# Optimization experiments

Hardware: AMD Instinct MI355X
Metric: run time of the kernel (lower is better)

The kernel has to match this reference:

```python
import jax, jax.numpy as jnp
import numpy as np

G, N, F, H, E = 3, 40000, 256, 128, 640000


def gcn_conv(x, W, b, edge_index):
    """PyG GCNConv: x @ W, add self-loops, sym-normalized scatter-add, + bias."""
    n = x.shape[0]
    x = x @ W
    loop = jnp.arange(n)
    row = jnp.concatenate([edge_index[0], loop])  # source nodes
    col = jnp.concatenate([edge_index[1], loop])  # target nodes
    deg = jax.ops.segment_sum(jnp.ones_like(row, dtype=x.dtype), col, num_segments=n)
    dinv = jnp.where(deg > 0, jax.lax.rsqrt(jnp.maximum(deg, 1e-12)), 0.0)
    norm = dinv[row] * dinv[col]
    out = jax.ops.segment_sum(x[row] * norm[:, None], col, num_segments=n)
    return out + b


def setup_inputs() -> dict:
    key = jax.random.key(0)
    ks = jax.random.split(key, 14)
    inp = {
        'x': jax.random.normal(ks[0], (G, N, F), jnp.float32),
        'edge_index': jax.random.randint(ks[1], (G, 2, E), 0, N, jnp.int64),
        'fc1_W': jax.random.normal(ks[2], (G, F, H), jnp.float32) * 0.05,
        'fc1_b': jax.random.normal(ks[3], (G, H), jnp.float32) * 0.05,
        'conv1_W': jax.random.normal(ks[4], (G, H, H), jnp.float32) * 0.05,
        'conv1_b': jax.random.normal(ks[5], (G, H), jnp.float32) * 0.05,
        'conv2_W': jax.random.normal(ks[6], (G, H, H), jnp.float32) * 0.05,
        'conv2_b': jax.random.normal(ks[7], (G, H), jnp.float32) * 0.05,
        'dconv1_W': jax.random.normal(ks[8], (G, H, H), jnp.float32) * 0.05,
        'dconv1_b': jax.random.normal(ks[9], (G, H), jnp.float32) * 0.05,
        'dconv2_W': jax.random.normal(ks[10], (G, H, H), jnp.float32) * 0.05,
        'dconv2_b': jax.random.normal(ks[11], (G, H), jnp.float32) * 0.05,
        'fc2_W': jax.random.normal(ks[12], (H, F), jnp.float32) * 0.05,
        'fc2_b': jax.random.normal(ks[13], (F,), jnp.float32) * 0.05,
    }
    return inp


def reference(x, edge_index, fc1_W, fc1_b, conv1_W, conv1_b, conv2_W, conv2_b,
              dconv1_W, dconv1_b, dconv2_W, dconv2_b, fc2_W, fc2_b):
    def encoder(xi, ei, fw, fb, c1w, c1b, c2w, c2b):
        pre = xi @ fw + fb                     # fc1
        h = gcn_conv(pre, c1w, c1b, ei)
        h = gcn_conv(h, c2w, c2b, ei)
        return pre, jax.nn.relu(h)

    pre_feat, enc = jax.vmap(encoder)(x, edge_index, fc1_W, fc1_b,
                                      conv1_W, conv1_b, conv2_W, conv2_b)

    # Faithful reproduction of the sequentially-mutating cross-graph block.
    h = [enc[i] for i in range(G)]
    for i in range(G):
        for j in range(G):
            if j != i:
                h[i] = h[i] + h[j]
        h[i] = h[G - 1] - h[i]  # loop var j ends at G-1 (zeroes tensor when i==G-1)
        h[i] = gcn_conv(h[i], dconv1_W[i], dconv1_b[i], edge_index[i])
        h[i] = gcn_conv(h[i], dconv2_W[i], dconv2_b[i], edge_index[i])

    fin_feat = h[0]
    for k in range(1, G - 1):
        fin_feat = fin_feat + h[k]

    loss_embedding = jax.nn.softmax(fin_feat @ fc2_W + fc2_b, axis=-1)
    return pre_feat, enc, jnp.stack(h), fin_feat, loss_embedding
```

## Files before the change

### kernel.cpp

```cpp
#include <hip/hip_runtime.h>
#include <hip/hip_bf16.h>

#define NV 40000
#define FD 256
#define HD 128
#define ED 640000
#define NG 3
#define NH (NV*HD)

#define CH  64
#define EPC (ED/CH)
#define NB  625

typedef unsigned short u16;
typedef unsigned int   u32;
typedef __attribute__((ext_vector_type(8))) u16    u16x8;
typedef __attribute__((ext_vector_type(8))) __bf16 bf16x8;
typedef __attribute__((ext_vector_type(4))) float  f32x4;

__device__ inline u16 f2b(float f){ __bf16 h = (__bf16)f; return __builtin_bit_cast(u16, h); }
__device__ inline float b2f(u16 u){ u32 x = ((u32)u)<<16; return __builtin_bit_cast(float, x); }
__device__ inline void acc2(u32 w, float&a, float&b){
  a += __builtin_bit_cast(float, w<<16);
  b += __builtin_bit_cast(float, w & 0xFFFF0000u);
}

__device__ inline void tr_seg(const float* __restrict__ src, u16* __restrict__ dst,
                              int K, int NN, long idx, long total){
  if (idx>=total) return;
  long per=(long)K*NN; long mat=idx/per; long rem=idx-mat*per;
  int k=(int)(rem/NN), c=(int)(rem-(long)k*NN);
  dst[mat*per+(long)c*K+k]=f2b(src[idx]);
}

__global__ __launch_bounds__(256) void htr_k(
    const int* __restrict__ ei, int* __restrict__ btot,
    const float* fc1W, const float* fc2W,
    const float* c1W, const float* c2W, const float* c1b,
    const float* d1W, const float* d2W, const float* d1b,
    u16* w_fc1, u16* w_fc2, u16* w_ce, u16* w_cd,
    float* t_enc, float* t_dec)
{
  __shared__ int h[NB];
  int b = blockIdx.x, t = threadIdx.x;
  if (b < 192){
    int ch = b % CH, g = b / CH;
    for (int i=t;i<NB;i+=256) h[i]=0;
    __syncthreads();
    const int* cc = ei + (long)g*2*ED + ED + ch*EPC;
    for (int j=t;j<EPC;j+=256) atomicAdd(&h[cc[j]>>6],1);
    __syncthreads();
    for (int bb=t;bb<NB;bb+=256){ int v=h[bb]; if(v) atomicAdd(&btot[g*NB+bb], v); }
    return;
  }
  int blk = b - 192;
  if (blk < 384){
    tr_seg(fc1W, w_fc1, FD, HD, (long)blk*256+t, (long)NG*FD*HD);
  } else if (blk < 512){
    tr_seg(fc2W, w_fc2, HD, FD, (long)(blk-384)*256+t, (long)HD*FD);
  } else if (blk < 832){
    int bb=blk-512;
    int mat=bb>>6;
    int local=(bb&63)*256+t;
    int n=local>>7, k=local&127;
    const float* W1; const float* W2; u16* dst;
    if (mat<3){ W1=c1W+(long)mat*HD*HD; W2=c2W+(long)mat*HD*HD; dst=w_ce+(long)mat*HD*HD; }
    else { int md=mat-3; W1=d1W+(long)md*HD*HD; W2=d2W+(long)md*HD*HD; dst=w_cd+(long)md*HD*HD; }
    float s=0.f;
    for (int j=0;j<HD;j++) s += W1[k*HD+j]*W2[j*HD+n];
    dst[(long)n*HD+k]=f2b(s);
  } else {
    for (int idx=t; idx<768; idx+=256){
      int which=idx>>7, n=idx&127;
      const float* bv; const float* W; float* dst;
      if (which<3){ bv=c1b+which*HD; W=c2W+(long)which*HD*HD; dst=t_enc+which*HD; }
      else { int w2=which-3; bv=d1b+w2*HD; W=d2W+(long)w2*HD*HD; dst=t_dec+w2*HD; }
      float s=0.f;
      for (int k=0;k<HD;k++) s += bv[k]*W[(long)k*HD+n];
      dst[n]=s;
    }
  }
}

__global__ void scanB_k(const int* __restrict__ btot, int* __restrict__ base, int* __restrict__ gcur){
  __shared__ int wsum[16];
  int tid=threadIdx.x, lane=tid&63, wv=tid>>6;
  for (int g=0; g<NG; ++g){
    int v = (tid<NB)? btot[g*NB+tid] : 0;
    int s=v;
    #pragma unroll
    for (int d=1; d<64; d<<=1){ int u=__shfl_up(s,d,64); if(lane>=d) s+=u; }
    if (lane==63) wsum[wv]=s;
    __syncthreads();
    if (wv==0){
      int t3=(lane<16)?wsum[lane]:0;
      #pragma unroll
      for (int d=1; d<16; d<<=1){ int u=__shfl_up(t3,d,64); if(lane>=d) t3+=u; }
      if (lane<16) wsum[lane]=t3;
    }
    __syncthreads();
    int incl = s + (wv>0? wsum[wv-1]:0);
    if (tid<NB){
      base[g*(NB+1)+tid]=incl-v;
      gcur[g*NB+tid]=incl-v;
      if (tid==NB-1) base[g*(NB+1)+NB]=incl;
    }
    __syncthreads();
  }
}

__global__ __launch_bounds__(256) void scat_k(const int* __restrict__ ei, int* __restrict__ gcur,
                                              u32* __restrict__ temp){
  int ch=blockIdx.x, g=blockIdx.y, t=threadIdx.x;
  __shared__ int h[NB];
  __shared__ int cur[NB];
  for (int i=t;i<NB;i+=256) h[i]=0;
  __syncthreads();
  const int* rr = ei + (long)g*2*ED + ch*EPC;
  const int* cc = rr + ED;
  for (int j=t;j<EPC;j+=256) atomicAdd(&h[cc[j]>>6],1);
  __syncthreads();
  for (int b=t;b<NB;b+=256){ int v=h[b]; cur[b] = v? atomicAdd(&gcur[g*NB+b], v) : 0; }
  __syncthreads();
  u32* tg = temp + (long)g*ED;
  for (int j=t;j<EPC;j+=256){
    int r=rr[j], c=cc[j];
    int pos=atomicAdd(&cur[c>>6],1);
    tg[pos]=((u32)(c&63)<<16)|(u32)r;
  }
}

__global__ __launch_bounds__(256) void sort_k(const u32* __restrict__ temp, const int* __restrict__ base,
                                              u16* __restrict__ csr, int* __restrict__ cptr,
                                              float* __restrict__ dinv){
  int b=blockIdx.x, g=blockIdx.y, t=threadIdx.x;
  __shared__ int cnt[64];
  __shared__ int cur[64];
  if (t<64) cnt[t]=0;
  __syncthreads();
  const u32* tg = temp + (long)g*ED;
  int s=base[g*(NB+1)+b], e=base[g*(NB+1)+b+1];
  for (int i=s+t;i<e;i+=256) atomicAdd(&cnt[tg[i]>>16],1);
  __syncthreads();
  if (t<64){
    int v=cnt[t];
    int sc=v;
    #pragma unroll
    for (int d=1;d<64;d<<=1){ int u=__shfl_up(sc,d,64); if(t>=d) sc+=u; }
    int st = s + sc - v;
    cur[t]=st;
    cptr[(long)g*(NV+1) + b*64 + t] = st;
    if (b==NB-1 && t==63) cptr[(long)g*(NV+1)+NV] = e;
    dinv[(long)g*NV + b*64 + t] = rsqrtf((float)v+1.0f);
  }
  __syncthreads();
  u16* cg = csr + (long)g*ED;
  for (int i=s+t;i<e;i+=256){
    u32 tt=tg[i];
    int pos=atomicAdd(&cur[tt>>16],1);
    cg[pos]=(u16)(tt&0xFFFF);
  }
}

__device__ __forceinline__ void agg_body(
    const u16* __restrict__ xw, const u16* __restrict__ csr,
    const int* __restrict__ cptr, const float* __restrict__ dinv,
    u16* __restrict__ outB, int c, int lane, int scOut)
{
  const uint2* xp2 = (const uint2*)xw;
  int hl = lane & 31;
  int hi = lane >> 5;
  float dc = dinv[c];
  float s0=0.f, s1=0.f, s2=0.f, s3=0.f;
  {
    uint2 v = xp2[(long)c*32 + hl];
    if (hi==0){ acc2(v.x, s0, s1); acc2(v.y, s2, s3); }
  }
  int j0 = cptr[c], j1 = cptr[c+1];
  int deg = j1 - j0;
  int idx = 0;
  if (lane < deg) idx = csr[j0 + lane];
  int nhc = min((deg+1)>>1, 32);
  int i = 0;
  for (; 2*i+7 < deg && i+4 <= nhc; i+=4){
    int p0=__shfl(idx, 2*i+hi,   64);
    int p1=__shfl(idx, 2*i+2+hi, 64);
    int p2=__shfl(idx, 2*i+4+hi, 64);
    int p3=__shfl(idx, 2*i+6+hi, 64);
    uint2 v0=xp2[(long)p0*32+hl], v1=xp2[(long)p1*32+hl];
    uint2 v2=xp2[(long)p2*32+hl], v3=xp2[(long)p3*32+hl];
    acc2(v0.x,s0,s1); acc2(v0.y,s2,s3);
    acc2(v1.x,s0,s1); acc2(v1.y,s2,s3);
    acc2(v2.x,s0,s1); acc2(v2.y,s2,s3);
    acc2(v3.x,s0,s1); acc2(v3.y,s2,s3);
  }
  for (; i<nhc; ++i){
    int e = 2*i+hi;
    int p = __shfl(idx, e<deg ? e : 0, 64);
    if (e < deg){
      uint2 v=xp2[(long)p*32+hl];
      acc2(v.x,s0,s1); acc2(v.y,s2,s3);
    }
  }
  if (deg > 64){
    int nt = deg - 64;
    int nth = (nt - hi + 1) >> 1;
    for (int i2=0; i2<nth; ++i2){
      int r = csr[j0 + 64 + 2*i2 + hi];
      uint2 v = xp2[(long)r*32+hl];
      acc2(v.x,s0,s1); acc2(v.y,s2,s3);
    }
  }
  s0 += __shfl_xor(s0,32,64);
  s1 += __shfl_xor(s1,32,64);
  s2 += __shfl_xor(s2,32,64);
  s3 += __shfl_xor(s3,32,64);
  if (hi==0){
    float m = scOut ? dc*dc : dc;
    u32 lo  = (u32)f2b(m*s0) | ((u32)f2b(m*s1)<<16);
    u32 hi2 = (u32)f2b(m*s2) | ((u32)f2b(m*s3)<<16);
    ((uint2*)outB)[(long)c*32 + hl] = make_uint2(lo, hi2);
  }
}

__device__ __forceinline__ void svec_body(
    const u16* __restrict__ csr, const int* __restrict__ cptr,
    const float* __restrict__ dinv, float* __restrict__ sv, int wid, int lane)
{
  int g = wid / NV, c = wid - g*NV;
  const u16* cg = csr + (long)g*ED;
  const int* cp = cptr + (long)g*(NV+1);
  const float* dv = dinv + (long)g*NV;
  int j0=cp[c], j1=cp[c+1];
  float sum=0.f;
  for (int j=j0+lane;j<j1;j+=64) sum+=dv[cg[j]];
  #pragma unroll
  for (int o=32;o;o>>=1) sum+=__shfl_xor(sum,o,64);
  if (lane==0){ float dc=dv[c]; sv[(long)g*NV+c]=dc*(dc+sum); }
}

__global__ __launch_bounds__(256) void agg_k(
    const u16* __restrict__ xw, const u16* __restrict__ csr,
    const int* __restrict__ cptr, const float* __restrict__ dinv,
    u16* __restrict__ outB, int scOut)
{
  int wid = blockIdx.x*4 + (threadIdx.x>>6);
  int g = wid / NV, c = wid - g*NV;
  agg_body(xw + (long)g*NH, csr + (long)g*ED, cptr + (long)g*(NV+1),
           dinv + (long)g*NV, outB + (long)g*NH, c, threadIdx.x & 63, scOut);
}

__global__ __launch_bounds__(256) void aggsv_k(
    const u16* __restrict__ xw, const u16* __restrict__ csr,
    const int* __restrict__ cptr, const float* __restrict__ dinv,
    u16* __restrict__ outB, int scOut, float* __restrict__ sv)
{
  int lane = threadIdx.x & 63;
  if (blockIdx.x < NG*NV/4){
    int wid = blockIdx.x*4 + (threadIdx.x>>6);
    int g = wid / NV, c = wid - g*NV;
    agg_body(xw + (long)g*NH, csr + (long)g*ED, cptr + (long)g*(NV+1),
             dinv + (long)g*NV, outB + (long)g*NH, c, lane, scOut);
  } else {
    int wid = (blockIdx.x - NG*NV/4)*4 + (threadIdx.x>>6);
    svec_body(csr, cptr, dinv, sv, wid, lane);
  }
}

template<int MODE, int EX>
__global__ __launch_bounds__(256) void gemm_k(
    const void* __restrict__ A_, long sA,
    const u16* __restrict__ Bt, long sB,
    const float* __restrict__ biasCol, long sBias,
    const float* __restrict__ svec, long sS,
    const float* __restrict__ tvec,
    const float* __restrict__ scaleRow, long sSc,
    const float* __restrict__ Add,
    float* __restrict__ Cf, long sCf,
    float* __restrict__ Cf2,
    u16* __restrict__ Cb, long sCb,
    int M, int N, int K, int relu)
{
  __shared__ __align__(16) u16 lsA[128*64];
  __shared__ __align__(16) u16 lsB[128*64];
  const int gz = blockIdx.z;
  const float* Af = (const float*)A_ + (long)gz*sA;
  const u16*   Ab = (const u16*)  A_ + (long)gz*sA;
  const u16* Bp = Bt + (long)gz*sB;
  const int t = threadIdx.x;
  const int lane = t & 63, wv = t >> 6, wm = wv >> 1, wn = wv & 1;
  const int lr = lane & 15, lq = lane >> 4;
  const int ar = t >> 1, ah = t & 1;
  const long grow = (long)blockIdx.x*128 + ar;
  const int colB = blockIdx.y*128 + ar;

  f32x4 acc[4][4];
  #pragma unroll
  for (int m=0;m<4;m++)
    #pragma unroll
    for (int n=0;n<4;n++) acc[m][n] = (f32x4)(0.0f);

  for (int k0=0; k0<K; k0+=64){
    if (k0) __syncthreads();
    u16x8 av[4];
    if (grow < M){
      if (MODE==0){
        const u16x8* s = (const u16x8*)(Ab + grow*(long)K + k0 + ah*32);
        #pragma unroll
        for (int i=0;i<4;i++) av[i] = s[i];
      } else {
        const float4* s = (const float4*)(Af + grow*(long)K + k0 + ah*32);
        #pragma unroll
        for (int i=0;i<4;i++){
          float4 v0 = s[i*2], v1 = s[i*2+1];
          u16x8 w;
          w[0]=f2b(v0.x); w[1]=f2b(v0.y); w[2]=f2b(v0.z); w[3]=f2b(v0.w);
          w[4]=f2b(v1.x); w[5]=f2b(v1.y); w[6]=f2b(v1.z); w[7]=f2b(v1.w);
          av[i] = w;
        }
      }
    } else {
      #pragma unroll
      for (int i=0;i<4;i++) av[i] = (u16x8)((u16)0);
    }
    #pragma unroll
    for (int i=0;i<4;i++){
      int q = ah*4 + i;
      *(u16x8*)&lsA[ar*64 + ((q ^ (ar&7))<<3)] = av[i];
    }
    {
      const u16x8* s = (const u16x8*)(Bp + (long)colB*K + k0 + ah*32);
      #pragma unroll
      for (int i=0;i<4;i++){
        int q = ah*4 + i;
        *(u16x8*)&lsB[ar*64 + ((q ^ (ar&7))<<3)] = s[i];
      }
    }
    __syncthreads();
    #pragma unroll
    for (int kk=0; kk<2; kk++){
      bf16x8 afr[4], bfr[4];
      #pragma unroll
      for (int m=0;m<4;m++){
        int r = wm*64 + m*16 + lr;
        int q = kk*4 + lq;
        afr[m] = __builtin_bit_cast(bf16x8, *(const u16x8*)&lsA[r*64 + ((q ^ (r&7))<<3)]);
      }
      #pragma unroll
      for (int n=0;n<4;n++){
        int r = wn*64 + n*16 + lr;
        int q = kk*4 + lq;
        bfr[n] = __builtin_bit_cast(bf16x8, *(const u16x8*)&lsB[r*64 + ((q ^ (r&7))<<3)]);
      }
      #pragma unroll
      for (int m=0;m<4;m++)
        #pragma unroll
        for (int n=0;n<4;n++)
          acc[m][n] = __builtin_amdgcn_mfma_f32_16x16x32_bf16(afr[m], bfr[n], acc[m][n], 0, 0, 0);
    }
  }
  #pragma unroll
  for (int m=0;m<4;m++){
    long gr0 = (long)blockIdx.x*128 + wm*64 + m*16 + lq*4;
    #pragma unroll
    for (int n=0;n<4;n++){
      int gc = blockIdx.y*128 + wn*64 + n*16 + lr;
      float bb = biasCol[gz*sBias + gc];
      float tv = (svec!=nullptr) ? tvec[gz*sBias + gc] : 0.0f;
      #pragma unroll
      for (int i=0;i<4;i++){
        long gr = gr0 + i;
        if (gr < M){
          float v = acc[m][n][i] + bb;
          if (svec!=nullptr) v += svec[gz*sS + gr]*tv;
          if (relu) v = fmaxf(v, 0.0f);
          if (EX==0){
            if (Cf) Cf[gz*sCf + gr*(long)N + gc] = v;
            if (Cb){
              float sc = scaleRow ? scaleRow[gz*sSc + gr] : 1.0f;
              Cb[gz*sCb + gr*(long)N + gc] = f2b(v*sc);
            }
          } else if (EX==1){
            Cf[gz*sCf + gr*(long)N + gc] = v;
            float z = -(v + Add[gr*(long)N + gc]) * scaleRow[gr];
            Cb[gz*sCb + gr*(long)N + gc] = f2b(z);
          } else {
            Cf[gz*sCf + gr*(long)N + gc] = v;
            float fv = v + Add[gr*(long)N + gc];
            Cf2[gr*(long)N + gc] = fv;
            if (Cb) Cb[gz*sCb + gr*(long)N + gc] = f2b(fv);
          }
        }
      }
    }
  }
}

__global__ void ewzh2_k(const float4* __restrict__ e0, const float4* __restrict__ e1,
                        const float* __restrict__ dinv0, u16* __restrict__ outB,
                        const float* __restrict__ sv2, const float* __restrict__ t2,
                        const float* __restrict__ b2, float4* __restrict__ outH2){
  int blk = blockIdx.x;
  if (blk < (NH/4)/256){
    int i = blk*256 + threadIdx.x;
    int row = i>>5;
    float d = dinv0[row];
    float4 a = e0[i], b = e1[i];
    float x0=-d*(a.x+b.x), x1=-d*(a.y+b.y), x2=-d*(a.z+b.z), x3=-d*(a.w+b.w);
    ((uint2*)outB)[i] = make_uint2((u32)f2b(x0) | ((u32)f2b(x1)<<16),
                                   (u32)f2b(x2) | ((u32)f2b(x3)<<16));
  } else {
    int i = (blk - (NH/4)/256)*256 + threadIdx.x;
    int row = i>>5, c4 = i&31;
    float s = sv2[row];
    float4 tv = ((const float4*)t2)[c4];
    float4 bb = ((const float4*)b2)[c4];
    outH2[i] = make_float4(s*tv.x+bb.x, s*tv.y+bb.y, s*tv.z+bb.z, s*tv.w+bb.w);
  }
}

__global__ __launch_bounds__(256) void fc2sm_k(
    const u16* __restrict__ Ab, const u16* __restrict__ Bw,
    const float* __restrict__ bias, float* __restrict__ Out, int M)
{
  __shared__ __align__(16) u16 lsA[128*64];
  __shared__ __align__(16) u16 lsB[256*64];
  const int t = threadIdx.x;
  const int lane = t & 63, wv = t >> 6, wm = wv >> 1, wn = wv & 1;
  const int lr = lane & 15, lq = lane >> 4;
  const int ar = t >> 1, ah = t & 1;
  const long grow = (long)blockIdx.x*128 + ar;

  f32x4 acc[4][8];
  #pragma unroll
  for (int m=0;m<4;m++)
    #pragma unroll
    for (int n=0;n<8;n++) acc[m][n] = (f32x4)(0.0f);

  for (int k0=0; k0<128; k0+=64){
    if (k0) __syncthreads();
    {
      u16x8 av[4];
      if (grow < M){
        const u16x8* s = (const u16x8*)(Ab + grow*128L + k0 + ah*32);
        #pragma unroll
        for (int i=0;i<4;i++) av[i] = s[i];
      } else {
        #pragma unroll
        for (int i=0;i<4;i++) av[i] = (u16x8)((u16)0);
      }
      #pragma unroll
      for (int i=0;i<4;i++){
        int q = ah*4 + i;
        *(u16x8*)&lsA[ar*64 + ((q ^ (ar&7))<<3)] = av[i];
      }
    }
    #pragma unroll
    for (int rr=0; rr<2; rr++){
      int r = ar + rr*128;
      const u16x8* s = (const u16x8*)(Bw + (long)r*128 + k0 + ah*32);
      #pragma unroll
      for (int i=0;i<4;i++){
        int q = ah*4 + i;
        *(u16x8*)&lsB[r*64 + ((q ^ (r&7))<<3)] = s[i];
      }
    }
    __syncthreads();
    #pragma unroll
    for (int kk=0; kk<2; kk++){
      bf16x8 afr[4], bfr[8];
      #pragma unroll
      for (int m=0;m<4;m++){
        int r = wm*64 + m*16 + lr;
        int q = kk*4 + lq;
        afr[m] = __builtin_bit_cast(bf16x8, *(const u16x8*)&lsA[r*64 + ((q ^ (r&7))<<3)]);
      }
      #pragma unroll
      for (int n=0;n<8;n++){
        int r = wn*128 + n*16 + lr;
        int q = kk*4 + lq;
        bfr[n] = __builtin_bit_cast(bf16x8, *(const u16x8*)&lsB[r*64 + ((q ^ (r&7))<<3)]);
      }
      #pragma unroll
      for (int m=0;m<4;m++)
        #pragma unroll
        for (int n=0;n<8;n++)
          acc[m][n] = __builtin_amdgcn_mfma_f32_16x16x32_bf16(afr[m], bfr[n], acc[m][n], 0, 0, 0);
    }
  }
  #pragma unroll
  for (int n=0;n<8;n++){
    float bb = bias[wn*128 + n*16 + lr];
    #pragma unroll
    for (int m=0;m<4;m++)
      #pragma unroll
      for (int i=0;i<4;i++) acc[m][n][i] += bb;
  }
  __syncthreads();
  float* lsF = (float*)lsA;
  #pragma unroll
  for (int m=0;m<4;m++)
    #pragma unroll
    for (int i=0;i<4;i++){
      float v = acc[m][0][i];
      #pragma unroll
      for (int n=1;n<8;n++) v = fmaxf(v, acc[m][n][i]);
      #pragma unroll
      for (int o=8;o;o>>=1) v = fmaxf(v, __shfl_xor(v, o, 16));
      if (lr==0) lsF[(wm*64 + m*16 + lq*4 + i)*2 + wn] = v;
    }
  __syncthreads();
  #pragma unroll
  for (int m=0;m<4;m++)
    #pragma unroll
    for (int i=0;i<4;i++){
      int rl = wm*64 + m*16 + lq*4 + i;
      float rm = fmaxf(lsF[rl*2], lsF[rl*2+1]);
      float s = 0.f;
      #pragma unroll
      for (int n=0;n<8;n++){
        float e = __expf(acc[m][n][i] - rm);
        acc[m][n][i] = e;
        s += e;
      }
      #pragma unroll
      for (int o=8;o;o>>=1) s += __shfl_xor(s, o, 16);
      if (lr==0) lsF[256 + rl*2 + wn] = s;
    }
  __syncthreads();
  #pragma unroll
  for (int m=0;m<4;m++){
    long gr0 = (long)blockIdx.x*128 + wm*64 + m*16 + lq*4;
    #pragma unroll
    for (int i=0;i<4;i++){
      long gr = gr0 + i;
      if (gr < M){
        int rl = wm*64 + m*16 + lq*4 + i;
        float inv = 1.0f/(lsF[256 + rl*2] + lsF[256 + rl*2 + 1]);
        #pragma unroll
        for (int n=0;n<8;n++){
          int gc = wn*128 + n*16 + lr;
          Out[gr*256L + gc] = acc[m][n][i]*inv;
        }
      }
    }
  }
}

extern "C" void kernel_launch(void* const* d_in, const int* in_sizes, int n_in,
                              void* d_out, int out_size, void* d_ws, size_t ws_size,
                              hipStream_t stream)
{
  const float* x    = (const float*)d_in[0];
  const int*   ei   = (const int*)  d_in[1];
  const float* fc1W = (const float*)d_in[2];
  const float* fc1b = (const float*)d_in[3];
  const float* c1W  = (const float*)d_in[4];
  const float* c1b  = (const float*)d_in[5];
  const float* c2W  = (const float*)d_in[6];
  const float* c2b  = (const float*)d_in[7];
  const float* d1W  = (const float*)d_in[8];
  const float* d1b  = (const float*)d_in[9];
  const float* d2W  = (const float*)d_in[10];
  const float* d2b  = (const float*)d_in[11];
  const float* fc2W = (const float*)d_in[12];
  const float* fc2b = (const float*)d_in[13];
  (void)in_sizes; (void)n_in; (void)out_size; (void)ws_size;

  float* out  = (float*)d_out;
  float* O_pre = out;
  float* O_enc = out + (long)NG*NH;
  float* O_h   = out + 2L*NG*NH;
  float* O_fin = out + 3L*NG*NH;
  float* O_ls  = O_fin + NH;

  char* p = (char*)d_ws;
  auto alloc = [&](size_t bytes)->void*{
    void* r = (void*)p; p += (bytes + 255) & ~(size_t)255; return r;
  };
  u16* bfA    = (u16*)alloc((size_t)NG*NH*2);
  u16* bfB    = (u16*)alloc((size_t)NG*NH*2);
  u16* bfC    = (u16*)alloc((size_t)NG*NH*2);
  u16* wt_fc1 = (u16*)alloc((size_t)NG*FD*HD*2);
  u16* wt_fc2 = (u16*)alloc((size_t)HD*FD*2);
  u16* wt_ce  = (u16*)alloc((size_t)NG*HD*HD*2);
  u16* wt_cd  = (u16*)alloc((size_t)2*HD*HD*2);
  float* t_enc = (float*)alloc((size_t)NG*HD*4);
  float* t_dec = (float*)alloc((size_t)NG*HD*4);
  u32*  temp  = (u32*) alloc((size_t)NG*ED*4);
  u16*  csr   = (u16*) alloc((size_t)NG*ED*2);
  int*  cptr  = (int*) alloc((size_t)NG*(NV+1)*4);
  int*  btot  = (int*) alloc((size_t)NG*NB*4);
  int*  base  = (int*) alloc((size_t)NG*(NB+1)*4);
  int*  gcur  = (int*) alloc((size_t)NG*NB*4);
  float* dinv = (float*)alloc((size_t)NG*NV*4);
  float* svec = (float*)alloc((size_t)NG*NV*4);

  hipMemsetAsync(btot, 0, (size_t)NG*NB*4, stream);
  htr_k<<<192+833, 256, 0, stream>>>(ei, btot, fc1W, fc2W, c1W, c2W, c1b, d1W, d2W, d1b,
                                     wt_fc1, wt_fc2, wt_ce, wt_cd, t_enc, t_dec);
  scanB_k<<<1, 1024, 0, stream>>>(btot, base, gcur);
  scat_k<<<dim3(CH,NG), 256, 0, stream>>>(ei, gcur, temp);
  sort_k<<<dim3(NB,NG), 256, 0, stream>>>(temp, base, csr, cptr, dinv);

  dim3 g3((NV+127)/128, 1, NG);
  dim3 g1((NV+127)/128, 1, 1);

  gemm_k<1,0><<<g3, 256, 0, stream>>>(x, (long)NV*FD, wt_fc1, (long)FD*HD, fc1b, HD,
                                      nullptr, 0, nullptr, dinv, NV, nullptr,
                                      O_pre, NH, nullptr, bfA, NH, NV, HD, FD, 0);

  aggsv_k<<<2*(NG*NV/4), 256, 0, stream>>>(bfA, csr, cptr, dinv, bfB, 1, svec);
  agg_k<<<NG*NV/4, 256, 0, stream>>>(bfB, csr, cptr, dinv, bfC, 0);

  gemm_k<0,0><<<g3, 256, 0, stream>>>(bfC, NH, wt_ce, (long)HD*HD, c2b, HD,
                                      svec, NV, t_enc, nullptr, 0, nullptr,
                                      O_enc, NH, nullptr, nullptr, 0, NV, HD, HD, 1);

  ewzh2_k<<<2*(NH/4)/256, 256, 0, stream>>>((const float4*)O_enc, (const float4*)(O_enc+NH), dinv, bfA,
                                            svec + 2L*NV, t_dec + 2*HD, d2b + 2*HD,
                                            (float4*)(O_h + 2L*NH));

  agg_k<<<NV/4, 256, 0, stream>>>(bfA, csr, cptr, dinv, bfB, 1);
  agg_k<<<NV/4, 256, 0, stream>>>(bfB, csr, cptr, dinv, bfC, 0);
  gemm_k<0,1><<<g1, 256, 0, stream>>>(bfC, 0, wt_cd, 0, d2b, 0,
                                      svec, 0, t_dec, dinv + NV, 0, O_enc + NH,
                                      O_h, 0, nullptr, bfA, 0, NV, HD, HD, 0);

  agg_k<<<NV/4, 256, 0, stream>>>(bfA, csr + ED, cptr + (NV+1), dinv + NV, bfB, 1);
  agg_k<<<NV/4, 256, 0, stream>>>(bfB, csr + ED, cptr + (NV+1), dinv + NV, bfC, 0);
  gemm_k<0,2><<<g1, 256, 0, stream>>>(bfC, 0, wt_cd + (long)HD*HD, 0, d2b + HD, 0,
                                      svec + NV, 0, t_dec + HD, nullptr, 0, O_h,
                                      O_h + NH, 0, O_fin, bfA, 0, NV, HD, HD, 0);

  fc2sm_k<<<(NV+127)/128, 256, 0, stream>>>(bfA, wt_fc2, fc2b, O_ls, NV);
}
```

Measured before the change: 589.2 us.

## Split GCN aggregation into four feature-column slice passes per node

New measurement: 947.7 us. 1.61x slower.

```diff
diff --git a/kernel.cpp b/kernel.cpp
--- a/kernel.cpp
+++ b/kernel.cpp
@@ -11,6 +11,7 @@
 #define CH  64
 #define EPC (ED/CH)
 #define NB  625
+#define BPS (NV/4)
 
 typedef unsigned short u16;
 typedef unsigned int   u32;
@@ -162,64 +163,54 @@
   }
 }
 
-__device__ __forceinline__ void agg_body(
+__device__ __forceinline__ void agg_slice_body(
     const u16* __restrict__ xw, const u16* __restrict__ csr,
     const int* __restrict__ cptr, const float* __restrict__ dinv,
-    u16* __restrict__ outB, int c, int lane, int scOut)
-{
-  const uint2* xp2 = (const uint2*)xw;
-  int hl = lane & 31;
-  int hi = lane >> 5;
+    u16* __restrict__ outB, int c, int lane, int scOut, int pass)
+{
+  const u32* xp = (const u32*)xw;
+  int q = lane >> 4;
+  int s = lane & 15;
+  long boff = (long)pass*16 + s;
   float dc = dinv[c];
-  float s0=0.f, s1=0.f, s2=0.f, s3=0.f;
-  {
-    uint2 v = xp2[(long)c*32 + hl];
-    if (hi==0){ acc2(v.x, s0, s1); acc2(v.y, s2, s3); }
+  float s0=0.f, s1=0.f;
+  if (q==0){
+    u32 v = xp[(long)c*64 + boff];
+    acc2(v, s0, s1);
   }
   int j0 = cptr[c], j1 = cptr[c+1];
   int deg = j1 - j0;
   int idx = 0;
   if (lane < deg) idx = csr[j0 + lane];
-  int nhc = min((deg+1)>>1, 32);
+  int nqc = min((deg+3)>>2, 16);
   int i = 0;
-  for (; 2*i+7 < deg && i+4 <= nhc; i+=4){
-    int p0=__shfl(idx, 2*i+hi,   64);
-    int p1=__shfl(idx, 2*i+2+hi, 64);
-    int p2=__shfl(idx, 2*i+4+hi, 64);
-    int p3=__shfl(idx, 2*i+6+hi, 64);
-    uint2 v0=xp2[(long)p0*32+hl], v1=xp2[(long)p1*32+hl];
-    uint2 v2=xp2[(long)p2*32+hl], v3=xp2[(long)p3*32+hl];
-    acc2(v0.x,s0,s1); acc2(v0.y,s2,s3);
-    acc2(v1.x,s0,s1); acc2(v1.y,s2,s3);
-    acc2(v2.x,s0,s1); acc2(v2.y,s2,s3);
-    acc2(v3.x,s0,s1); acc2(v3.y,s2,s3);
-  }
-  for (; i<nhc; ++i){
-    int e = 2*i+hi;
+  for (; 4*i+7 < deg && i+2 <= nqc; i+=2){
+    int p0 = __shfl(idx, 4*i+q,   64);
+    int p1 = __shfl(idx, 4*i+4+q, 64);
+    u32 v0 = xp[(long)p0*64 + boff];
+    u32 v1 = xp[(long)p1*64 + boff];
+    acc2(v0,s0,s1); acc2(v1,s0,s1);
+  }
+  for (; i<nqc; ++i){
+    int e = 4*i+q;
     int p = __shfl(idx, e<deg ? e : 0, 64);
     if (e < deg){
-      uint2 v=xp2[(long)p*32+hl];
-      acc2(v.x,s0,s1); acc2(v.y,s2,s3);
+      u32 v = xp[(long)p*64 + boff];
+      acc2(v,s0,s1);
     }
   }
   if (deg > 64){
-    int nt = deg - 64;
-    int nth = (nt - hi + 1) >> 1;
-    for (int i2=0; i2<nth; ++i2){
-      int r = csr[j0 + 64 + 2*i2 + hi];
-      uint2 v = xp2[(long)r*32+hl];
-      acc2(v.x,s0,s1); acc2(v.y,s2,s3);
-    }
-  }
-  s0 += __shfl_xor(s0,32,64);
-  s1 += __shfl_xor(s1,32,64);
-  s2 += __shfl_xor(s2,32,64);
-  s3 += __shfl_xor(s3,32,64);
-  if (hi==0){
+    for (int e = 64+q; e < deg; e += 4){
+      int r = csr[j0+e];
+      u32 v = xp[(long)r*64 + boff];
+      acc2(v,s0,s1);
+    }
+  }
+  s0 += __shfl_xor(s0,16,64); s0 += __shfl_xor(s0,32,64);
+  s1 += __shfl_xor(s1,16,64); s1 += __shfl_xor(s1,32,64);
+  if (q==0){
     float m = scOut ? dc*dc : dc;
-    u32 lo  = (u32)f2b(m*s0) | ((u32)f2b(m*s1)<<16);
-    u32 hi2 = (u32)f2b(m*s2) | ((u32)f2b(m*s3)<<16);
-    ((uint2*)outB)[(long)c*32 + hl] = make_uint2(lo, hi2);
+    ((u32*)outB)[(long)c*64 + boff] = (u32)f2b(m*s0) | ((u32)f2b(m*s1)<<16);
   }
 }
 
@@ -239,30 +230,35 @@
   if (lane==0){ float dc=dv[c]; sv[(long)g*NV+c]=dc*(dc+sum); }
 }
 
-__global__ __launch_bounds__(256) void agg_k(
+__global__ __launch_bounds__(256) void aggp_k(
     const u16* __restrict__ xw, const u16* __restrict__ csr,
     const int* __restrict__ cptr, const float* __restrict__ dinv,
-    u16* __restrict__ outB, int scOut)
-{
-  int wid = blockIdx.x*4 + (threadIdx.x>>6);
-  int g = wid / NV, c = wid - g*NV;
-  agg_body(xw + (long)g*NH, csr + (long)g*ED, cptr + (long)g*(NV+1),
-           dinv + (long)g*NV, outB + (long)g*NH, c, threadIdx.x & 63, scOut);
-}
-
-__global__ __launch_bounds__(256) void aggsv_k(
+    u16* __restrict__ outB, int scOut, int ng)
+{
+  int wv = threadIdx.x >> 6, lane = threadIdx.x & 63;
+  int sb = blockIdx.x / BPS;
+  int nb = blockIdx.x - sb*BPS;
+  int pass = sb / ng, g = sb - pass*ng;
+  int c = nb*4 + wv;
+  agg_slice_body(xw + (long)g*NH, csr + (long)g*ED, cptr + (long)g*(NV+1),
+                 dinv + (long)g*NV, outB + (long)g*NH, c, lane, scOut, pass);
+}
+
+__global__ __launch_bounds__(256) void aggsvp_k(
     const u16* __restrict__ xw, const u16* __restrict__ csr,
     const int* __restrict__ cptr, const float* __restrict__ dinv,
     u16* __restrict__ outB, int scOut, float* __restrict__ sv)
 {
-  int lane = threadIdx.x & 63;
-  if (blockIdx.x < NG*NV/4){
-    int wid = blockIdx.x*4 + (threadIdx.x>>6);
-    int g = wid / NV, c = wid - g*NV;
-    agg_body(xw + (long)g*NH, csr + (long)g*ED, cptr + (long)g*(NV+1),
-             dinv + (long)g*NV, outB + (long)g*NH, c, lane, scOut);
+  int wv = threadIdx.x >> 6, lane = threadIdx.x & 63;
+  if (blockIdx.x < 4*NG*BPS){
+    int sb = blockIdx.x / BPS;
+    int nb = blockIdx.x - sb*BPS;
+    int pass = sb / NG, g = sb - pass*NG;
+    int c = nb*4 + wv;
+    agg_slice_body(xw + (long)g*NH, csr + (long)g*ED, cptr + (long)g*(NV+1),
+                   dinv + (long)g*NV, outB + (long)g*NH, c, lane, scOut, pass);
   } else {
-    int wid = (blockIdx.x - NG*NV/4)*4 + (threadIdx.x>>6);
+    int wid = (blockIdx.x - 4*NG*BPS)*4 + wv;
     svec_body(csr, cptr, dinv, sv, wid, lane);
   }
 }
@@ -610,8 +606,8 @@
                                       nullptr, 0, nullptr, dinv, NV, nullptr,
                                       O_pre, NH, nullptr, bfA, NH, NV, HD, FD, 0);
 
-  aggsv_k<<<2*(NG*NV/4), 256, 0, stream>>>(bfA, csr, cptr, dinv, bfB, 1, svec);
-  agg_k<<<NG*NV/4, 256, 0, stream>>>(bfB, csr, cptr, dinv, bfC, 0);
+  aggsvp_k<<<4*NG*BPS + NG*NV/4, 256, 0, stream>>>(bfA, csr, cptr, dinv, bfB, 1, svec);
+  aggp_k<<<4*NG*BPS, 256, 0, stream>>>(bfB, csr, cptr, dinv, bfC, 0, NG);
 
   gemm_k<0,0><<<g3, 256, 0, stream>>>(bfC, NH, wt_ce, (long)HD*HD, c2b, HD,
                                       svec, NV, t_enc, nullptr, 0, nullptr,
@@ -621,14 +617,14 @@
                                             svec + 2L*NV, t_dec + 2*HD, d2b + 2*HD,
                                             (float4*)(O_h + 2L*NH));
 
-  agg_k<<<NV/4, 256, 0, stream>>>(bfA, csr, cptr, dinv, bfB, 1);
-  agg_k<<<NV/4, 256, 0, stream>>>(bfB, csr, cptr, dinv, bfC, 0);
+  aggp_k<<<4*BPS, 256, 0, stream>>>(bfA, csr, cptr, dinv, bfB, 1, 1);
+  aggp_k<<<4*BPS, 256, 0, stream>>>(bfB, csr, cptr, dinv, bfC, 0, 1);
   gemm_k<0,1><<<g1, 256, 0, stream>>>(bfC, 0, wt_cd, 0, d2b, 0,
                                       svec, 0, t_dec, dinv + NV, 0, O_enc + NH,
                                       O_h, 0, nullptr, bfA, 0, NV, HD, HD, 0);
 
-  agg_k<<<NV/4, 256, 0, stream>>>(bfA, csr + ED, cptr + (NV+1), dinv + NV, bfB, 1);
-  agg_k<<<NV/4, 256, 0, stream>>>(bfB, csr + ED, cptr + (NV+1), dinv + NV, bfC, 0);
+  aggp_k<<<4*BPS, 256, 0, stream>>>(bfA, csr + ED, cptr + (NV+1), dinv + NV, bfB, 1, 1);
+  aggp_k<<<4*BPS, 256, 0, stream>>>(bfB, csr + ED, cptr + (NV+1), dinv + NV, bfC, 0, 1);
   gemm_k<0,2><<<g1, 256, 0, stream>>>(bfC, 0, wt_cd + (long)HD*HD, 0, d2b + HD, 0,
                                       svec + NV, 0, t_dec + HD, nullptr, 0, O_h,
                                       O_h + NH, 0, O_fin, bfA, 0, NV, HD, HD, 0);
```
